# Performance work log

Measured on AMD Instinct MI355X. Metric: run time of the kernel, lower is better.

Reference implementation:

```python
import jax, jax.numpy as jnp
import numpy as np

N = 50000
E = 1_600_000
D_IN = 128
D_H = 64
D_E = 32
NEG_SLOPE = 0.2


def setup_inputs() -> dict:
    key = jax.random.key(0)
    ks = jax.random.split(key, 20)
    p = lambda k, sh: jax.random.normal(k, sh, jnp.float32) * 0.1
    return {
        "x": jax.random.normal(ks[0], (N, D_IN), jnp.float32),
        "edge_index": jax.random.randint(ks[1], (2, E), 0, N, jnp.int32),
        "edge_attr": jax.random.normal(ks[2], (E, D_E), jnp.float32),
        # layer 1 params (GATv2Conv, heads=1)
        "Wl1": p(ks[3], (D_IN, D_H)), "bl1": p(ks[4], (D_H,)),
        "Wr1": p(ks[5], (D_IN, D_H)), "br1": p(ks[6], (D_H,)),
        "We1": p(ks[7], (D_E, D_H)),
        "att1": p(ks[8], (D_H,)), "bias1": p(ks[9], (D_H,)),
        # layer 2 params
        "Wl2": p(ks[10], (D_H, D_H)), "bl2": p(ks[11], (D_H,)),
        "Wr2": p(ks[12], (D_H, D_H)), "br2": p(ks[13], (D_H,)),
        "We2": p(ks[14], (D_E, D_H)),
        "att2": p(ks[15], (D_H,)), "bias2": p(ks[16], (D_H,)),
        # classifier
        "Wc": p(ks[17], (D_H, 2)), "bc": p(ks[18], (2,)),
    }


def _gatv2(x, src, dst, eattr, Wl, bl, Wr, br, We, att, bias, n):
    # x: [n, d_in]; src/dst: [Ea]; eattr: [Ea, d_e]
    xl = x @ Wl + bl                      # [n, d_h] (source transform; also message value)
    xr = x @ Wr + br                      # [n, d_h] (target transform)
    z = xl[src] + xr[dst] + eattr @ We    # [Ea, d_h]
    score = jax.nn.leaky_relu(z, NEG_SLOPE) @ att  # [Ea]
    # numerically stable softmax over incoming edges per destination node
    m = jax.ops.segment_max(score, dst, num_segments=n)
    ex = jnp.exp(score - m[dst])
    denom = jax.ops.segment_sum(ex, dst, num_segments=n)
    alpha = ex / denom[dst]               # [Ea]
    out = jax.ops.segment_sum(alpha[:, None] * xl[src], dst, num_segments=n)
    return out + bias


def reference(x, edge_index, edge_attr,
              Wl1, bl1, Wr1, br1, We1, att1, bias1,
              Wl2, bl2, Wr2, br2, We2, att2, bias2,
              Wc, bc):
    n = x.shape[0]
    src, dst = edge_index[0], edge_index[1]
    # add self-loops with fill_value='mean' (PyG default with edge_attr):
    # self-loop edge feature of node i = mean of edge_attr over edges into i
    e = edge_attr.shape[0]
    deg = jax.ops.segment_sum(jnp.ones((e,), edge_attr.dtype), dst, num_segments=n)
    loop_attr = jax.ops.segment_sum(edge_attr, dst, num_segments=n) / jnp.maximum(deg, 1.0)[:, None]
    loop = jnp.arange(n, dtype=edge_index.dtype)
    src_a = jnp.concatenate([src, loop])
    dst_a = jnp.concatenate([dst, loop])
    ea = jnp.concatenate([edge_attr, loop_attr], axis=0)

    h = jax.nn.relu(_gatv2(x, src_a, dst_a, ea, Wl1, bl1, Wr1, br1, We1, att1, bias1, n))
    # dropout(p=0.2) is identity in eval mode
    h = jax.nn.relu(_gatv2(h, src_a, dst_a, ea, Wl2, bl2, Wr2, br2, We2, att2, bias2, n))
    return h @ Wc + bc  # [n, 2]
```

## Files before the change

### kernel.cpp

```cpp
#include <hip/hip_runtime.h>
#include <hip/hip_bf16.h>

#define NEG_SLOPE 0.2f

typedef __attribute__((ext_vector_type(8))) short bf16x8;
typedef __attribute__((ext_vector_type(4))) float f32x4;

__device__ __forceinline__ float bf2f(unsigned short u) {
    return __uint_as_float((unsigned)u << 16);
}
__device__ __forceinline__ float bflo(unsigned u) { return __uint_as_float(u << 16); }
__device__ __forceinline__ float bfhi(unsigned u) { return __uint_as_float(u & 0xFFFF0000u); }
__device__ __forceinline__ unsigned short f2bf(float f) {
    unsigned b = __float_as_uint(f);
    return (unsigned short)((b + 0x7FFFu + ((b >> 16) & 1u)) >> 16);
}

__global__ void k_hist(const int* __restrict__ dst, int E, int* __restrict__ deg) {
    int e = blockIdx.x * 256 + threadIdx.x;
    if (e < E) atomicAdd(&deg[dst[e]], 1);
}

__global__ __launch_bounds__(1024) void k_scan_chunk(const int* __restrict__ deg,
                                                     int* __restrict__ start,
                                                     int* __restrict__ csum, int n) {
    __shared__ int wsum[16];
    const int lane = threadIdx.x & 63;
    const int w = threadIdx.x >> 6;
    int i = blockIdx.x * 1024 + (int)threadIdx.x;
    int v = (i < n) ? deg[i] : 0;
    int s = v;
#pragma unroll
    for (int o = 1; o < 64; o <<= 1) {
        int u = __shfl_up(s, o);
        if (lane >= o) s += u;
    }
    if (lane == 63) wsum[w] = s;
    __syncthreads();
    if (w == 0) {
        int ws = (lane < 16) ? wsum[lane] : 0;
#pragma unroll
        for (int o = 1; o < 16; o <<= 1) {
            int u = __shfl_up(ws, o);
            if (lane >= o) ws += u;
        }
        if (lane < 16) wsum[lane] = ws;
    }
    __syncthreads();
    int woff = (w == 0) ? 0 : wsum[w - 1];
    int incl = s + woff;
    if (i < n) start[i] = incl - v;
    if (threadIdx.x == 1023) csum[blockIdx.x] = incl;
}

__global__ void k_scan_top(int* __restrict__ csum, int nch, int* __restrict__ start, int n) {
    int t = threadIdx.x;
    int v = (t < nch) ? csum[t] : 0;
    int s = v;
#pragma unroll
    for (int o = 1; o < 64; o <<= 1) {
        int u = __shfl_up(s, o);
        if (t >= o) s += u;
    }
    if (t < nch) csum[t] = s - v;
    if (t == 63) start[n] = s;
}

__global__ void k_scan_apply(int* __restrict__ start, const int* __restrict__ csum, int n) {
    int i = blockIdx.x * 256 + threadIdx.x;
    if (i < n) start[i] += csum[i >> 10];
}

__global__ void k_fill(const int* __restrict__ src, const int* __restrict__ dst, int E,
                       const int* __restrict__ start, int* __restrict__ cursor,
                       int2* __restrict__ es_sorted, int* __restrict__ sortpos) {
    int e = blockIdx.x * 256 + threadIdx.x;
    if (e >= E) return;
    int d = dst[e];
    int idx = start[d] + atomicAdd(&cursor[d], 1);
    es_sorted[idx] = make_int2(e, src[e]);
    sortpos[e] = idx;
}

__global__ __launch_bounds__(256) void k_loop_csr(
    const float* __restrict__ eattr, const int2* __restrict__ es_sorted,
    const int* __restrict__ start, float* __restrict__ loop_attr, int n) {
    int node = blockIdx.x * 4 + (threadIdx.x >> 6);
    int t = threadIdx.x & 63;
    if (node >= n) return;
    int a = start[node], b = start[node + 1];
    int g = t >> 3, gl = t & 7;
    float4 acc = make_float4(0.f, 0.f, 0.f, 0.f);
    int j = a + g;
    for (; j + 8 < b; j += 16) {
        int e1 = es_sorted[j].x;
        int e2 = es_sorted[j + 8].x;
        const float4 v1 = *(const float4*)&eattr[(size_t)e1 * 32 + gl * 4];
        const float4 v2 = *(const float4*)&eattr[(size_t)e2 * 32 + gl * 4];
        acc.x += v1.x + v2.x; acc.y += v1.y + v2.y;
        acc.z += v1.z + v2.z; acc.w += v1.w + v2.w;
    }
    if (j < b) {
        int e = es_sorted[j].x;
        const float4 v = *(const float4*)&eattr[(size_t)e * 32 + gl * 4];
        acc.x += v.x; acc.y += v.y; acc.z += v.z; acc.w += v.w;
    }
#pragma unroll
    for (int mask = 8; mask <= 32; mask <<= 1) {
        acc.x += __shfl_xor(acc.x, mask);
        acc.y += __shfl_xor(acc.y, mask);
        acc.z += __shfl_xor(acc.z, mask);
        acc.w += __shfl_xor(acc.w, mask);
    }
    if (t < 8) {
        float deg = fmaxf((float)(b - a), 1.f);
        float4 o = make_float4(acc.x / deg, acc.y / deg, acc.z / deg, acc.w / deg);
        *(float4*)&loop_attr[(size_t)node * 32 + gl * 4] = o;
    }
}

template <int DIN>
__global__ void k_node_transform(const float* __restrict__ h,
                                 const float* __restrict__ Wl, const float* __restrict__ bl,
                                 const float* __restrict__ Wr, const float* __restrict__ br,
                                 unsigned short* __restrict__ xlb,
                                 unsigned short* __restrict__ xrb, int n) {
    __shared__ float hs[4][DIN];
    int node0 = blockIdx.x * 4;
    int tid = threadIdx.x;
    for (int idx = tid; idx < 4 * DIN; idx += 256) {
        int ln = idx / DIN, k = idx % DIN;
        int node = node0 + ln;
        hs[ln][k] = (node < n) ? h[(long long)node * DIN + k] : 0.f;
    }
    __syncthreads();
    int ln = tid >> 6;
    int j = tid & 63;
    int node = node0 + ln;
    if (node >= n) return;
    float al = bl[j], ar = br[j];
#pragma unroll 8
    for (int k = 0; k < DIN; ++k) {
        float hv = hs[ln][k];
        al += hv * Wl[k * 64 + j];
        ar += hv * Wr[k * 64 + j];
    }
    xlb[(long long)node * 64 + j] = f2bf(al);
    xrb[(long long)node * 64 + j] = f2bf(ar);
}

__global__ __launch_bounds__(256, 2) void k_edge_score(
    const unsigned short* __restrict__ xlb, const unsigned short* __restrict__ xrb,
    const float* __restrict__ eattr,
    const float* __restrict__ We, const float* __restrict__ att,
    const int* __restrict__ src, const int* __restrict__ dst,
    const int* __restrict__ sortpos, int E,
    float* __restrict__ ex_sorted) {
    __shared__ __align__(16) short ea_frag[4][128][8];

    const int tid = threadIdx.x;
    const int ge0 = blockIdx.x * 128;
    const int w = tid >> 6, l = tid & 63;
    const int lo16 = l & 15, hi4 = l >> 4;

    int sq[2], dq[2];
#pragma unroll
    for (int et = 0; et < 2; ++et) {
        int ge = ge0 + w * 32 + et * 16 + lo16;
        bool ok = ge < E;
        sq[et] = ok ? src[ge] : 0;
        dq[et] = ok ? dst[ge] : 0;
    }
    uint4 xlg[2][2], xrg[2][2];
#pragma unroll
    for (int et = 0; et < 2; ++et) {
        const size_t lbase = (size_t)sq[et] * 64 + hi4 * 16;
        const size_t rbase = (size_t)dq[et] * 64 + hi4 * 16;
        xlg[et][0] = *(const uint4*)&xlb[lbase];
        xlg[et][1] = *(const uint4*)&xlb[lbase + 8];
        xrg[et][0] = *(const uint4*)&xrb[rbase];
        xrg[et][1] = *(const uint4*)&xrb[rbase + 8];
    }

    {
        const int e = tid & 127;
        const int c0 = (tid >> 7) * 2;
        const int ge = ge0 + e;
        float4 a = make_float4(0.f, 0.f, 0.f, 0.f), b = a, c = a, d4 = a;
        if (ge < E) {
            const float4* p = (const float4*)(eattr + (size_t)ge * 32 + c0 * 8);
            a = p[0]; b = p[1]; c = p[2]; d4 = p[3];
        }
        bf16x8 lo, hi;
        lo[0] = (short)f2bf(a.x); lo[1] = (short)f2bf(a.y); lo[2] = (short)f2bf(a.z); lo[3] = (short)f2bf(a.w);
        lo[4] = (short)f2bf(b.x); lo[5] = (short)f2bf(b.y); lo[6] = (short)f2bf(b.z); lo[7] = (short)f2bf(b.w);
        hi[0] = (short)f2bf(c.x); hi[1] = (short)f2bf(c.y); hi[2] = (short)f2bf(c.z); hi[3] = (short)f2bf(c.w);
        hi[4] = (short)f2bf(d4.x); hi[5] = (short)f2bf(d4.y); hi[6] = (short)f2bf(d4.z); hi[7] = (short)f2bf(d4.w);
        *(bf16x8*)&ea_frag[c0 + 0][e][0] = lo;
        *(bf16x8*)&ea_frag[c0 + 1][e][0] = hi;
    }

    bf16x8 afrag[4];
#pragma unroll
    for (int ct = 0; ct < 4; ++ct) {
        const int ch = (lo16 >> 2) * 16 + ct * 4 + (lo16 & 3);
#pragma unroll
        for (int j = 0; j < 8; ++j) {
            afrag[ct][j] = (short)f2bf(We[(hi4 * 8 + j) * 64 + ch]);
        }
    }
    float attf[16];
    {
        const float4 a0 = *(const float4*)&att[hi4 * 16 + 0];
        const float4 a1 = *(const float4*)&att[hi4 * 16 + 4];
        const float4 a2 = *(const float4*)&att[hi4 * 16 + 8];
        const float4 a3 = *(const float4*)&att[hi4 * 16 + 12];
        attf[0] = a0.x;  attf[1] = a0.y;  attf[2] = a0.z;  attf[3] = a0.w;
        attf[4] = a1.x;  attf[5] = a1.y;  attf[6] = a1.z;  attf[7] = a1.w;
        attf[8] = a2.x;  attf[9] = a2.y;  attf[10] = a2.z; attf[11] = a2.w;
        attf[12] = a3.x; attf[13] = a3.y; attf[14] = a3.z; attf[15] = a3.w;
    }
    __syncthreads();

    f32x4 acc[2][4];
#pragma unroll
    for (int et = 0; et < 2; ++et) {
        bf16x8 bfrag = *(const bf16x8*)&ea_frag[hi4][w * 32 + et * 16 + lo16][0];
#pragma unroll
        for (int ct = 0; ct < 4; ++ct) {
            f32x4 zero = {0.f, 0.f, 0.f, 0.f};
            acc[et][ct] = __builtin_amdgcn_mfma_f32_16x16x32_bf16(afrag[ct], bfrag, zero, 0, 0, 0);
        }
    }

#pragma unroll
    for (int et = 0; et < 2; ++et) {
        float xlf[16], xrf[16];
#pragma unroll
        for (int h = 0; h < 2; ++h) {
            const uint4 ql = xlg[et][h];
            const uint4 qr = xrg[et][h];
            xlf[h * 8 + 0] = bflo(ql.x); xlf[h * 8 + 1] = bfhi(ql.x);
            xlf[h * 8 + 2] = bflo(ql.y); xlf[h * 8 + 3] = bfhi(ql.y);
            xlf[h * 8 + 4] = bflo(ql.z); xlf[h * 8 + 5] = bfhi(ql.z);
            xlf[h * 8 + 6] = bflo(ql.w); xlf[h * 8 + 7] = bfhi(ql.w);
            xrf[h * 8 + 0] = bflo(qr.x); xrf[h * 8 + 1] = bfhi(qr.x);
            xrf[h * 8 + 2] = bflo(qr.y); xrf[h * 8 + 3] = bfhi(qr.y);
            xrf[h * 8 + 4] = bflo(qr.z); xrf[h * 8 + 5] = bfhi(qr.z);
            xrf[h * 8 + 6] = bflo(qr.w); xrf[h * 8 + 7] = bfhi(qr.w);
        }
        float part = 0.f;
#pragma unroll
        for (int ct = 0; ct < 4; ++ct) {
#pragma unroll
            for (int r = 0; r < 4; ++r) {
                const int i = ct * 4 + r;
                float zz = acc[et][ct][r] + xlf[i] + xrf[i];
                zz = (zz > 0.f) ? zz : NEG_SLOPE * zz;
                part += attf[i] * zz;
            }
        }
        part += __shfl_xor(part, 16);
        part += __shfl_xor(part, 32);
        if (l < 16) {
            int ge = ge0 + w * 32 + et * 16 + l;
            if (ge < E) ex_sorted[sortpos[ge]] = __expf(part);
        }
    }
}

template <bool FINAL>
__global__ __launch_bounds__(256, 2) void k_node_aggr(
    const unsigned short* __restrict__ xlb, const unsigned short* __restrict__ xrb,
    const float* __restrict__ loop_attr,
    const float* __restrict__ We, const float* __restrict__ att,
    const int* __restrict__ start,
    const int2* __restrict__ es_sorted, const float* __restrict__ ex_sorted,
    const float* __restrict__ bias,
    const float* __restrict__ Wc, const float* __restrict__ bc,
    float* __restrict__ hout, int n) {
    __shared__ float la_s[4][32];
    const int ln = threadIdx.x >> 6;
    const int node = blockIdx.x * 4 + ln;
    const int t = threadIdx.x & 63;

    if (threadIdx.x < 128) {
        int nn = blockIdx.x * 4 + (threadIdx.x >> 5);
        int k = threadIdx.x & 31;
        la_s[threadIdx.x >> 5][k] = (nn < n) ? loop_attr[(size_t)nn * 32 + k] : 0.f;
    }
    __syncthreads();
    if (node >= n) return;

    float exl;
    {
        float zl = bf2f(xlb[(size_t)node * 64 + t]) + bf2f(xrb[(size_t)node * 64 + t]);
#pragma unroll 8
        for (int k = 0; k < 32; ++k) zl += We[k * 64 + t] * la_s[ln][k];
        zl = (zl > 0.f) ? zl : NEG_SLOPE * zl;
        float v = att[t] * zl;
#pragma unroll
        for (int mask = 1; mask <= 32; mask <<= 1) v += __shfl_xor(v, mask);
        exl = __expf(v);
    }

    const int g = t >> 3;
    const int c8 = t & 7;
    int a = start[node], b = start[node + 1];

    float acc[8] = {0.f, 0.f, 0.f, 0.f, 0.f, 0.f, 0.f, 0.f};
    float den = 0.f;
    if (g == 0) {
        const uint4 q = *(const uint4*)&xlb[(size_t)node * 64 + c8 * 8];
        acc[0] = exl * bflo(q.x); acc[1] = exl * bfhi(q.x);
        acc[2] = exl * bflo(q.y); acc[3] = exl * bfhi(q.y);
        acc[4] = exl * bflo(q.z); acc[5] = exl * bfhi(q.z);
        acc[6] = exl * bflo(q.w); acc[7] = exl * bfhi(q.w);
        den = exl;
    }
    for (int j = a; j < b; j += 64) {
        int m = b - j; if (m > 64) m = 64;
        int sj = 0; float exj = 0.f;
        if (t < m) { sj = es_sorted[j + t].y; exj = ex_sorted[j + t]; }
        for (int i = 0; i < m; i += 16) {
            const int i0 = i + g, i1 = i + 8 + g;
            const int s0 = __shfl(sj, i0); const float e0 = __shfl(exj, i0);
            const int s1 = __shfl(sj, i1); const float e1 = __shfl(exj, i1);
            uint4 q0 = *(const uint4*)&xlb[(size_t)s0 * 64 + c8 * 8];
            uint4 q1 = *(const uint4*)&xlb[(size_t)s1 * 64 + c8 * 8];
            if (i0 < m) {
                acc[0] += e0 * bflo(q0.x); acc[1] += e0 * bfhi(q0.x);
                acc[2] += e0 * bflo(q0.y); acc[3] += e0 * bfhi(q0.y);
                acc[4] += e0 * bflo(q0.z); acc[5] += e0 * bfhi(q0.z);
                acc[6] += e0 * bflo(q0.w); acc[7] += e0 * bfhi(q0.w);
                den += e0;
            }
            if (i1 < m) {
                acc[0] += e1 * bflo(q1.x); acc[1] += e1 * bfhi(q1.x);
                acc[2] += e1 * bflo(q1.y); acc[3] += e1 * bfhi(q1.y);
                acc[4] += e1 * bflo(q1.z); acc[5] += e1 * bfhi(q1.z);
                acc[6] += e1 * bflo(q1.w); acc[7] += e1 * bfhi(q1.w);
                den += e1;
            }
        }
    }
#pragma unroll
    for (int mask = 8; mask <= 32; mask <<= 1) {
#pragma unroll
        for (int r = 0; r < 8; ++r) acc[r] += __shfl_xor(acc[r], mask);
        den += __shfl_xor(den, mask);
    }
    if (!FINAL) {
        if (g == 0) {
            float h[8];
#pragma unroll
            for (int r = 0; r < 8; ++r)
                h[r] = fmaxf(acc[r] / den + bias[c8 * 8 + r], 0.f);
            float4 o0 = make_float4(h[0], h[1], h[2], h[3]);
            float4 o1 = make_float4(h[4], h[5], h[6], h[7]);
            *(float4*)&hout[(size_t)node * 64 + c8 * 8] = o0;
            *(float4*)&hout[(size_t)node * 64 + c8 * 8 + 4] = o1;
        }
    } else {
        float v0 = 0.f, v1 = 0.f;
        if (g == 0) {
#pragma unroll
            for (int r = 0; r < 8; ++r) {
                const int ch = c8 * 8 + r;
                const float h = fmaxf(acc[r] / den + bias[ch], 0.f);
                v0 += h * Wc[ch * 2 + 0];
                v1 += h * Wc[ch * 2 + 1];
            }
        }
#pragma unroll
        for (int mask = 1; mask <= 4; mask <<= 1) {
            v0 += __shfl_xor(v0, mask);
            v1 += __shfl_xor(v1, mask);
        }
        if (t == 0) {
            hout[(size_t)node * 2 + 0] = v0 + bc[0];
            hout[(size_t)node * 2 + 1] = v1 + bc[1];
        }
    }
}

extern "C" void kernel_launch(void* const* d_in, const int* in_sizes, int n_in,
                              void* d_out, int out_size, void* d_ws, size_t ws_size,
                              hipStream_t stream) {
    const float* x     = (const float*)d_in[0];
    const int*   ei    = (const int*)d_in[1];
    const float* eattr = (const float*)d_in[2];
    const float* Wl1 = (const float*)d_in[3];
    const float* bl1 = (const float*)d_in[4];
    const float* Wr1 = (const float*)d_in[5];
    const float* br1 = (const float*)d_in[6];
    const float* We1 = (const float*)d_in[7];
    const float* att1 = (const float*)d_in[8];
    const float* bias1 = (const float*)d_in[9];
    const float* Wl2 = (const float*)d_in[10];
    const float* bl2 = (const float*)d_in[11];
    const float* Wr2 = (const float*)d_in[12];
    const float* br2 = (const float*)d_in[13];
    const float* We2 = (const float*)d_in[14];
    const float* att2 = (const float*)d_in[15];
    const float* bias2 = (const float*)d_in[16];
    const float* Wc = (const float*)d_in[17];
    const float* bc = (const float*)d_in[18];

    const int N = in_sizes[0] / 128;
    const int E = in_sizes[1] / 2;
    const int* src = ei;
    const int* dst = ei + E;

    char* w = (char*)d_ws;
    auto alloc = [&](size_t bytes) {
        char* p = w;
        w += (bytes + 255) & ~(size_t)255;
        return p;
    };
    unsigned short* xlb        = (unsigned short*)alloc((size_t)N * 64 * 2);
    unsigned short* xrb        = (unsigned short*)alloc((size_t)N * 64 * 2);
    float*          hbuf       = (float*)alloc((size_t)N * 64 * 4);
    float*          loop_attr  = (float*)alloc((size_t)N * 32 * 4);
    int*            deg_i      = (int*)alloc((size_t)N * 4);
    int*            start      = (int*)alloc((size_t)(N + 1) * 4);
    int*            cursor     = (int*)alloc((size_t)N * 4);
    int*            csum       = (int*)alloc(256 * 4);
    int2*           es_sorted  = (int2*)alloc((size_t)E * 8);
    int*            sortpos    = (int*)alloc((size_t)E * 4);
    float*          ex_sorted  = (float*)alloc((size_t)E * 4);

    const int THREADS = 256;
    const int score_blocks = (E + 127) / 128;
    const int node4_blocks = (N + 3) / 4;
    const int edge_blocks = (E + THREADS - 1) / THREADS;
    const int nchunks = (N + 1023) / 1024;

    hipMemsetAsync(deg_i, 0, (size_t)N * 4, stream);
    hipMemsetAsync(cursor, 0, (size_t)N * 4, stream);
    k_hist<<<edge_blocks, THREADS, 0, stream>>>(dst, E, deg_i);
    k_scan_chunk<<<nchunks, 1024, 0, stream>>>(deg_i, start, csum, N);
    k_scan_top<<<1, 64, 0, stream>>>(csum, nchunks, start, N);
    k_scan_apply<<<(N + THREADS - 1) / THREADS, THREADS, 0, stream>>>(start, csum, N);
    k_fill<<<edge_blocks, THREADS, 0, stream>>>(src, dst, E, start, cursor,
                                                es_sorted, sortpos);
    k_loop_csr<<<node4_blocks, THREADS, 0, stream>>>(eattr, es_sorted, start, loop_attr, N);

    k_node_transform<128><<<node4_blocks, THREADS, 0, stream>>>(x, Wl1, bl1, Wr1, br1,
                                                                xlb, xrb, N);
    k_edge_score<<<score_blocks, THREADS, 0, stream>>>(
        xlb, xrb, eattr, We1, att1, src, dst, sortpos, E, ex_sorted);
    k_node_aggr<false><<<node4_blocks, THREADS, 0, stream>>>(
        xlb, xrb, loop_attr, We1, att1, start, es_sorted, ex_sorted,
        bias1, Wc, bc, hbuf, N);

    k_node_transform<64><<<node4_blocks, THREADS, 0, stream>>>(hbuf, Wl2, bl2, Wr2, br2,
                                                               xlb, xrb, N);
    k_edge_score<<<score_blocks, THREADS, 0, stream>>>(
        xlb, xrb, eattr, We2, att2, src, dst, sortpos, E, ex_sorted);
    k_node_aggr<true><<<node4_blocks, THREADS, 0, stream>>>(
        xlb, xrb, loop_attr, We2, att2, start, es_sorted, ex_sorted,
        bias2, Wc, bc, (float*)d_out, N);
}
```

Baseline: 721.2 us.

## Pre-sort edge attributes as bf16 by destination and score edges in CSR order

k_fill now scatters each edge's attributes, converted to bf16, into destination-sorted order along with packed (src,dst) pairs. Edge scoring then runs in sorted order, reading half-width contiguous attributes and writing exponentials coalesced without the sortpos indirection. The self-loop mean also reads the sorted bf16 array contiguously. The cost is an extra E×64-byte scatter write in the preprocessing kernel, and the loop mean is now computed from bf16-rounded values.

Result: faster. 631.8 us (median of 2 runs) (-12.4%).

```diff
diff --git a/kernel.cpp b/kernel.cpp
--- a/kernel.cpp
+++ b/kernel.cpp
@@ -14,6 +14,9 @@
 __device__ __forceinline__ unsigned short f2bf(float f) {
     unsigned b = __float_as_uint(f);
     return (unsigned short)((b + 0x7FFFu + ((b >> 16) & 1u)) >> 16);
+}
+__device__ __forceinline__ unsigned pack2(float lo, float hi) {
+    return (unsigned)f2bf(lo) | ((unsigned)f2bf(hi) << 16);
 }
 
 __global__ void k_hist(const int* __restrict__ dst, int E, int* __restrict__ deg) {
@@ -71,51 +74,50 @@
     if (i < n) start[i] += csum[i >> 10];
 }
 
-__global__ void k_fill(const int* __restrict__ src, const int* __restrict__ dst, int E,
+__global__ void k_fill(const float* __restrict__ eattr,
+                       const int* __restrict__ src, const int* __restrict__ dst, int E,
                        const int* __restrict__ start, int* __restrict__ cursor,
-                       int2* __restrict__ es_sorted, int* __restrict__ sortpos) {
+                       int2* __restrict__ sd_sorted, unsigned short* __restrict__ eattr_s) {
     int e = blockIdx.x * 256 + threadIdx.x;
     if (e >= E) return;
     int d = dst[e];
     int idx = start[d] + atomicAdd(&cursor[d], 1);
-    es_sorted[idx] = make_int2(e, src[e]);
-    sortpos[e] = idx;
+    sd_sorted[idx] = make_int2(src[e], d);
+    const float4* p = (const float4*)(eattr + (size_t)e * 32);
+    uint4* q = (uint4*)(eattr_s + (size_t)idx * 32);
+#pragma unroll
+    for (int c = 0; c < 4; ++c) {
+        const float4 a = p[2 * c], b = p[2 * c + 1];
+        uint4 o;
+        o.x = pack2(a.x, a.y); o.y = pack2(a.z, a.w);
+        o.z = pack2(b.x, b.y); o.w = pack2(b.z, b.w);
+        q[c] = o;
+    }
 }
 
 __global__ __launch_bounds__(256) void k_loop_csr(
-    const float* __restrict__ eattr, const int2* __restrict__ es_sorted,
-    const int* __restrict__ start, float* __restrict__ loop_attr, int n) {
+    const unsigned short* __restrict__ eattr_s, const int* __restrict__ start,
+    float* __restrict__ loop_attr, int n) {
     int node = blockIdx.x * 4 + (threadIdx.x >> 6);
     int t = threadIdx.x & 63;
     if (node >= n) return;
     int a = start[node], b = start[node + 1];
-    int g = t >> 3, gl = t & 7;
-    float4 acc = make_float4(0.f, 0.f, 0.f, 0.f);
-    int j = a + g;
-    for (; j + 8 < b; j += 16) {
-        int e1 = es_sorted[j].x;
-        int e2 = es_sorted[j + 8].x;
-        const float4 v1 = *(const float4*)&eattr[(size_t)e1 * 32 + gl * 4];
-        const float4 v2 = *(const float4*)&eattr[(size_t)e2 * 32 + gl * 4];
-        acc.x += v1.x + v2.x; acc.y += v1.y + v2.y;
-        acc.z += v1.z + v2.z; acc.w += v1.w + v2.w;
-    }
-    if (j < b) {
-        int e = es_sorted[j].x;
-        const float4 v = *(const float4*)&eattr[(size_t)e * 32 + gl * 4];
-        acc.x += v.x; acc.y += v.y; acc.z += v.z; acc.w += v.w;
-    }
-#pragma unroll
-    for (int mask = 8; mask <= 32; mask <<= 1) {
-        acc.x += __shfl_xor(acc.x, mask);
-        acc.y += __shfl_xor(acc.y, mask);
-        acc.z += __shfl_xor(acc.z, mask);
-        acc.w += __shfl_xor(acc.w, mask);
-    }
-    if (t < 8) {
+    const int rpi = t >> 4;
+    const int cp = t & 15;
+    float ax = 0.f, ay = 0.f;
+    for (int j = a + rpi; j < b; j += 4) {
+        unsigned u = *(const unsigned*)&eattr_s[(size_t)j * 32 + cp * 2];
+        ax += bflo(u); ay += bfhi(u);
+    }
+#pragma unroll
+    for (int mask = 16; mask <= 32; mask <<= 1) {
+        ax += __shfl_xor(ax, mask);
+        ay += __shfl_xor(ay, mask);
+    }
+    if (t < 16) {
         float deg = fmaxf((float)(b - a), 1.f);
-        float4 o = make_float4(acc.x / deg, acc.y / deg, acc.z / deg, acc.w / deg);
-        *(float4*)&loop_attr[(size_t)node * 32 + gl * 4] = o;
+        float2 o = make_float2(ax / deg, ay / deg);
+        *(float2*)&loop_attr[(size_t)node * 32 + cp * 2] = o;
     }
 }
 
@@ -151,10 +153,9 @@
 
 __global__ __launch_bounds__(256, 2) void k_edge_score(
     const unsigned short* __restrict__ xlb, const unsigned short* __restrict__ xrb,
-    const float* __restrict__ eattr,
+    const unsigned short* __restrict__ eattr_s,
     const float* __restrict__ We, const float* __restrict__ att,
-    const int* __restrict__ src, const int* __restrict__ dst,
-    const int* __restrict__ sortpos, int E,
+    const int2* __restrict__ sd_sorted, int E,
     float* __restrict__ ex_sorted) {
     __shared__ __align__(16) short ea_frag[4][128][8];
 
@@ -163,19 +164,17 @@
     const int w = tid >> 6, l = tid & 63;
     const int lo16 = l & 15, hi4 = l >> 4;
 
-    int sq[2], dq[2];
+    int2 sd[2];
 #pragma unroll
     for (int et = 0; et < 2; ++et) {
         int ge = ge0 + w * 32 + et * 16 + lo16;
-        bool ok = ge < E;
-        sq[et] = ok ? src[ge] : 0;
-        dq[et] = ok ? dst[ge] : 0;
+        sd[et] = (ge < E) ? sd_sorted[ge] : make_int2(0, 0);
     }
     uint4 xlg[2][2], xrg[2][2];
 #pragma unroll
     for (int et = 0; et < 2; ++et) {
-        const size_t lbase = (size_t)sq[et] * 64 + hi4 * 16;
-        const size_t rbase = (size_t)dq[et] * 64 + hi4 * 16;
+        const size_t lbase = (size_t)sd[et].x * 64 + hi4 * 16;
+        const size_t rbase = (size_t)sd[et].y * 64 + hi4 * 16;
         xlg[et][0] = *(const uint4*)&xlb[lbase];
         xlg[et][1] = *(const uint4*)&xlb[lbase + 8];
         xrg[et][0] = *(const uint4*)&xrb[rbase];
@@ -186,18 +185,13 @@
         const int e = tid & 127;
         const int c0 = (tid >> 7) * 2;
         const int ge = ge0 + e;
-        float4 a = make_float4(0.f, 0.f, 0.f, 0.f), b = a, c = a, d4 = a;
+        uint4 q0 = make_uint4(0, 0, 0, 0), q1 = q0;
         if (ge < E) {
-            const float4* p = (const float4*)(eattr + (size_t)ge * 32 + c0 * 8);
-            a = p[0]; b = p[1]; c = p[2]; d4 = p[3];
-        }
-        bf16x8 lo, hi;
-        lo[0] = (short)f2bf(a.x); lo[1] = (short)f2bf(a.y); lo[2] = (short)f2bf(a.z); lo[3] = (short)f2bf(a.w);
-        lo[4] = (short)f2bf(b.x); lo[5] = (short)f2bf(b.y); lo[6] = (short)f2bf(b.z); lo[7] = (short)f2bf(b.w);
-        hi[0] = (short)f2bf(c.x); hi[1] = (short)f2bf(c.y); hi[2] = (short)f2bf(c.z); hi[3] = (short)f2bf(c.w);
-        hi[4] = (short)f2bf(d4.x); hi[5] = (short)f2bf(d4.y); hi[6] = (short)f2bf(d4.z); hi[7] = (short)f2bf(d4.w);
-        *(bf16x8*)&ea_frag[c0 + 0][e][0] = lo;
-        *(bf16x8*)&ea_frag[c0 + 1][e][0] = hi;
+            const uint4* p = (const uint4*)(eattr_s + (size_t)ge * 32 + c0 * 8);
+            q0 = p[0]; q1 = p[1];
+        }
+        *(uint4*)&ea_frag[c0 + 0][e][0] = q0;
+        *(uint4*)&ea_frag[c0 + 1][e][0] = q1;
     }
 
     bf16x8 afrag[4];
@@ -264,7 +258,7 @@
         part += __shfl_xor(part, 32);
         if (l < 16) {
             int ge = ge0 + w * 32 + et * 16 + l;
-            if (ge < E) ex_sorted[sortpos[ge]] = __expf(part);
+            if (ge < E) ex_sorted[ge] = __expf(part);
         }
     }
 }
@@ -275,7 +269,7 @@
     const float* __restrict__ loop_attr,
     const float* __restrict__ We, const float* __restrict__ att,
     const int* __restrict__ start,
-    const int2* __restrict__ es_sorted, const float* __restrict__ ex_sorted,
+    const int2* __restrict__ sd_sorted, const float* __restrict__ ex_sorted,
     const float* __restrict__ bias,
     const float* __restrict__ Wc, const float* __restrict__ bc,
     float* __restrict__ hout, int n) {
@@ -321,7 +315,7 @@
     for (int j = a; j < b; j += 64) {
         int m = b - j; if (m > 64) m = 64;
         int sj = 0; float exj = 0.f;
-        if (t < m) { sj = es_sorted[j + t].y; exj = ex_sorted[j + t]; }
+        if (t < m) { sj = sd_sorted[j + t].x; exj = ex_sorted[j + t]; }
         for (int i = 0; i < m; i += 16) {
             const int i0 = i + g, i1 = i + 8 + g;
             const int s0 = __shfl(sj, i0); const float e0 = __shfl(exj, i0);
@@ -426,9 +420,9 @@
     int*            start      = (int*)alloc((size_t)(N + 1) * 4);
     int*            cursor     = (int*)alloc((size_t)N * 4);
     int*            csum       = (int*)alloc(256 * 4);
-    int2*           es_sorted  = (int2*)alloc((size_t)E * 8);
-    int*            sortpos    = (int*)alloc((size_t)E * 4);
+    int2*           sd_sorted  = (int2*)alloc((size_t)E * 8);
     float*          ex_sorted  = (float*)alloc((size_t)E * 4);
+    unsigned short* eattr_s    = (unsigned short*)alloc((size_t)E * 32 * 2);
 
     const int THREADS = 256;
     const int score_blocks = (E + 127) / 128;
@@ -442,23 +436,23 @@
     k_scan_chunk<<<nchunks, 1024, 0, stream>>>(deg_i, start, csum, N);
     k_scan_top<<<1, 64, 0, stream>>>(csum, nchunks, start, N);
     k_scan_apply<<<(N + THREADS - 1) / THREADS, THREADS, 0, stream>>>(start, csum, N);
-    k_fill<<<edge_blocks, THREADS, 0, stream>>>(src, dst, E, start, cursor,
-                                                es_sorted, sortpos);
-    k_loop_csr<<<node4_blocks, THREADS, 0, stream>>>(eattr, es_sorted, start, loop_attr, N);
+    k_fill<<<edge_blocks, THREADS, 0, stream>>>(eattr, src, dst, E, start, cursor,
+                                                sd_sorted, eattr_s);
+    k_loop_csr<<<node4_blocks, THREADS, 0, stream>>>(eattr_s, start, loop_attr, N);
 
     k_node_transform<128><<<node4_blocks, THREADS, 0, stream>>>(x, Wl1, bl1, Wr1, br1,
                                                                 xlb, xrb, N);
     k_edge_score<<<score_blocks, THREADS, 0, stream>>>(
-        xlb, xrb, eattr, We1, att1, src, dst, sortpos, E, ex_sorted);
+        xlb, xrb, eattr_s, We1, att1, sd_sorted, E, ex_sorted);
     k_node_aggr<false><<<node4_blocks, THREADS, 0, stream>>>(
-        xlb, xrb, loop_attr, We1, att1, start, es_sorted, ex_sorted,
+        xlb, xrb, loop_attr, We1, att1, start, sd_sorted, ex_sorted,
         bias1, Wc, bc, hbuf, N);
 
     k_node_transform<64><<<node4_blocks, THREADS, 0, stream>>>(hbuf, Wl2, bl2, Wr2, br2,
                                                                xlb, xrb, N);
     k_edge_score<<<score_blocks, THREADS, 0, stream>>>(
-        xlb, xrb, eattr, We2, att2, src, dst, sortpos, E, ex_sorted);
+        xlb, xrb, eattr_s, We2, att2, sd_sorted, E, ex_sorted);
     k_node_aggr<true><<<node4_blocks, THREADS, 0, stream>>>(
-        xlb, xrb, loop_attr, We2, att2, start, es_sorted, ex_sorted,
+        xlb, xrb, loop_attr, We2, att2, start, sd_sorted, ex_sorted,
         bias2, Wc, bc, (float*)d_out, N);
 }
```
